# Optimization experiments

Measured on AMD Instinct MI355X. Metric: run time of the kernel, lower is better.

Reference implementation:

```python
import jax, jax.numpy as jnp
import numpy as np

H = 16        # query heads
K = 4         # kv heads (GQA)
D = 128       # head_dim
HID = 2048    # hidden_size
T = 2048      # num tokens (single prefill sequence, causal)
THETA = 10000.0


def setup_inputs() -> dict:
    key = jax.random.key(0)
    k1, k2, k3 = jax.random.split(key, 3)
    hidden_states = jax.random.normal(k1, (T, HID), dtype=jnp.float32)
    position_ids = jnp.arange(T, dtype=jnp.int32)
    Wqkv = jax.random.normal(k2, (HID, (H + 2 * K) * D), dtype=jnp.float32) * 0.02
    Wo = jax.random.normal(k3, (H * D, HID), dtype=jnp.float32) * 0.02
    return {"hidden_states": hidden_states, "position_ids": position_ids,
            "Wqkv": Wqkv, "Wo": Wo}


def _rope_neox(x, pos):
    # x: [T, heads, D]; neox style: rotate halves
    half = D // 2
    inv_freq = 1.0 / (THETA ** (jnp.arange(0, D, 2, dtype=jnp.float32) / D))  # [D/2]
    ang = pos.astype(jnp.float32)[:, None] * inv_freq                          # [T, D/2]
    cos = jnp.cos(ang)[:, None, :]
    sin = jnp.sin(ang)[:, None, :]
    x1, x2 = x[..., :half], x[..., half:]
    return jnp.concatenate([x1 * cos - x2 * sin, x2 * cos + x1 * sin], axis=-1)


def reference(hidden_states, position_ids, Wqkv, Wo):
    t = hidden_states.shape[0]
    qkv = hidden_states @ Wqkv                                   # [T, (H+2K)*D]
    q = qkv[:, : H * D].reshape(t, H, D)
    k = qkv[:, H * D : (H + K) * D].reshape(t, K, D)
    v = qkv[:, (H + K) * D :].reshape(t, K, D)
    q = _rope_neox(q, position_ids)
    k = _rope_neox(k, position_ids)
    # GQA: expand kv heads to H
    rep = H // K
    k = jnp.repeat(k, rep, axis=1)                               # [T, H, D]
    v = jnp.repeat(v, rep, axis=1)
    scale = D ** -0.5
    scores = jnp.einsum('qhd,khd->hqk', q, k) * scale            # [H, T, T]
    causal = jnp.arange(t)[:, None] >= jnp.arange(t)[None, :]    # [T, T]
    scores = jnp.where(causal[None], scores, jnp.finfo(scores.dtype).min)
    probs = jax.nn.softmax(scores, axis=-1)
    ctx = jnp.einsum('hqk,khd->qhd', probs, v).reshape(t, H * D)  # [T, H*D]
    return ctx @ Wo                                              # [T, HID]
```

## Files before the change

kernel.cpp:

```cpp
#include <hip/hip_runtime.h>
#include <hip/hip_bf16.h>
#include <stdint.h>

typedef __hip_bfloat16 bf16;
typedef __attribute__((ext_vector_type(8))) short bh8;
typedef __attribute__((ext_vector_type(4))) float f32x4;

#define MFMA16(a, b, c) __builtin_amdgcn_mfma_f32_16x16x32_bf16((a), (b), (c), 0, 0, 0)

typedef const __attribute__((address_space(1))) void* gas1_t;
typedef __attribute__((address_space(3))) void* las3_t;

__device__ __forceinline__ void gload_lds16(const void* g, void* l) {
  __builtin_amdgcn_global_load_lds((gas1_t)g, (las3_t)l, 16, 0, 0);
}

__device__ __forceinline__ float bfu2f(unsigned short u) {
  union { unsigned int i; float f; } c;
  c.i = (unsigned int)u << 16;
  return c.f;
}

__global__ __launch_bounds__(256) void cast_f32_bf16(const float* __restrict__ x,
                                                     bf16* __restrict__ y, int n4) {
  int i = blockIdx.x * 256 + threadIdx.x;
  if (i >= n4) return;
  float4 v = ((const float4*)x)[i];
  union { ushort4 u; bf16 b[4]; } o;
  o.b[0] = __float2bfloat16(v.x);
  o.b[1] = __float2bfloat16(v.y);
  o.b[2] = __float2bfloat16(v.z);
  o.b[3] = __float2bfloat16(v.w);
  ((ushort4*)y)[i] = o.u;
}

__global__ __launch_bounds__(256) void transpose_cast(const float* __restrict__ W,
                                                      bf16* __restrict__ WT, int R, int C) {
  __shared__ float tile[32][33];
  const int tx = threadIdx.x & 31, ty = threadIdx.x >> 5;
  const int bx = blockIdx.x, by = blockIdx.y;
#pragma unroll
  for (int p = 0; p < 4; ++p)
    tile[ty + p * 8][tx] = W[(long)(by * 32 + ty + p * 8) * C + bx * 32 + tx];
  __syncthreads();
#pragma unroll
  for (int p = 0; p < 4; ++p)
    WT[(long)(bx * 32 + ty + p * 8) * R + by * 32 + tx] = __float2bfloat16(tile[tx][ty + p * 8]);
}

template <bool BF16OUT>
__global__ __launch_bounds__(256) void gemm_bt_sk(const bf16* __restrict__ A,
                                                  const bf16* __restrict__ BT,
                                                  void* __restrict__ C0, void* __restrict__ C1,
                                                  int M, int N, int Kd, int nKs) {
  __shared__ bf16 As[128 * 64];
  __shared__ bf16 Bs[128 * 64];
  const int tid = threadIdx.x, lane = tid & 63, wid = tid >> 6;
  const int wr = wid >> 1, wc = wid & 1;
  const int bx = blockIdx.x, by = blockIdx.y, z = blockIdx.z;

  f32x4 acc[4][4];
#pragma unroll
  for (int m = 0; m < 4; ++m)
#pragma unroll
    for (int n = 0; n < 4; ++n)
#pragma unroll
      for (int r = 0; r < 4; ++r) acc[m][n][r] = 0.0f;

  const long Abase = (long)(by * 128) * Kd;
  const long Bbase = (long)(bx * 128) * Kd;
  const int lr = lane & 15, lh = lane >> 4;
  const int k00 = z * nKs * 64;

  for (int kt = 0; kt < nKs; ++kt) {
    __syncthreads();
    const int k0 = k00 + kt * 64;
#pragma unroll
    for (int i = 0; i < 4; ++i) {
      const int cb = i * 256 + wid * 64;
      const int c = cb + lane;
      const int row = c >> 3, s = c & 7;
      gload_lds16(A + Abase + (long)row * Kd + k0 + (s ^ (row & 7)) * 8, (char*)As + cb * 16);
      gload_lds16(BT + Bbase + (long)row * Kd + k0 + (s ^ (row & 7)) * 8, (char*)Bs + cb * 16);
    }
    __syncthreads();

#pragma unroll
    for (int kk = 0; kk < 2; ++kk) {
      bh8 af[4], bfv[4];
#pragma unroll
      for (int m = 0; m < 4; ++m)
        af[m] = *(const bh8*)((const char*)As +
                              (((wr * 64 + m * 16 + lr) * 128 + kk * 64 + lh * 16) ^
                               ((lr & 7) << 4)));
#pragma unroll
      for (int n = 0; n < 4; ++n)
        bfv[n] = *(const bh8*)((const char*)Bs +
                               (((wc * 64 + n * 16 + lr) * 128 + kk * 64 + lh * 16) ^
                                ((lr & 7) << 4)));
#pragma unroll
      for (int m = 0; m < 4; ++m)
#pragma unroll
        for (int n = 0; n < 4; ++n) acc[m][n] = MFMA16(af[m], bfv[n], acc[m][n]);
    }
  }

  const int r0 = by * 128 + wr * 64, c0 = bx * 128 + wc * 64;
  const int lrow = lh * 4;
  if (BF16OUT) {
    bf16* P = (bf16*)(z == 0 ? C0 : C1);
#pragma unroll
    for (int m = 0; m < 4; ++m)
#pragma unroll
      for (int n = 0; n < 4; ++n)
#pragma unroll
        for (int r = 0; r < 4; ++r)
          P[(long)(r0 + m * 16 + lrow + r) * N + c0 + n * 16 + lr] =
              __float2bfloat16(acc[m][n][r]);
  } else {
    float* P = (float*)(z == 0 ? C0 : C1);
#pragma unroll
    for (int m = 0; m < 4; ++m)
#pragma unroll
      for (int n = 0; n < 4; ++n)
#pragma unroll
        for (int r = 0; r < 4; ++r)
          P[(long)(r0 + m * 16 + lrow + r) * N + c0 + n * 16 + lr] = acc[m][n][r];
  }
}

__global__ __launch_bounds__(256) void out_reduce(float* __restrict__ out,
                                                  const float* __restrict__ p1, int n4) {
  int i = blockIdx.x * 256 + threadIdx.x;
  if (i >= n4) return;
  float4 a = ((const float4*)out)[i];
  float4 b = ((const float4*)p1)[i];
  a.x += b.x; a.y += b.y; a.z += b.z; a.w += b.w;
  ((float4*)out)[i] = a;
}

__global__ __launch_bounds__(256) void rope_split(const bf16* __restrict__ P0,
                                                  const bf16* __restrict__ P1,
                                                  const int* __restrict__ pos_ids,
                                                  bf16* __restrict__ Qb, bf16* __restrict__ Kb,
                                                  bf16* __restrict__ VbT) {
  const int t = blockIdx.x;
  const int tid = threadIdx.x;
  const float pos = (float)pos_ids[t];
  const float qscale = 0.08838834764831845f;
  const ushort* r0 = (const ushort*)(P0 + (long)t * 3072);
  const ushort* r1 = (const ushort*)(P1 + (long)t * 3072);
  for (int i = tid; i < 512; i += 256) {
    const int kvh = i >> 7, d = i & 127;
    const float v = bfu2f(r0[2560 + i]) + bfu2f(r1[2560 + i]);
    VbT[(long)(kvh * 128 + d) * 2048 + t] = __float2bfloat16(v);
  }
  for (int i = tid; i < 1280; i += 256) {
    const int hh = i >> 6, d = i & 63;
    const float inv = exp2f((float)d * -0.2076205059304594f);
    const float ang = pos * inv;
    const float c = cosf(ang), s = sinf(ang);
    const float x1 = bfu2f(r0[hh * 128 + d]) + bfu2f(r1[hh * 128 + d]);
    const float x2 = bfu2f(r0[hh * 128 + d + 64]) + bfu2f(r1[hh * 128 + d + 64]);
    const float o1 = x1 * c - x2 * s, o2 = x2 * c + x1 * s;
    if (hh < 16) {
      Qb[(long)t * 2048 + hh * 128 + d] = __float2bfloat16(o1 * qscale);
      Qb[(long)t * 2048 + hh * 128 + d + 64] = __float2bfloat16(o2 * qscale);
    } else {
      Kb[t * 512 + (hh - 16) * 128 + d] = __float2bfloat16(o1);
      Kb[t * 512 + (hh - 16) * 128 + d + 64] = __float2bfloat16(o2);
    }
  }
}

__global__ __launch_bounds__(256, 2) void attn_partial(const bf16* __restrict__ Qb,
                                                       const bf16* __restrict__ Kb,
                                                       const bf16* __restrict__ VbT,
                                                       bf16* __restrict__ Pctx,
                                                       float* __restrict__ ML) {
  const int h = blockIdx.x;
  const int qb = 31 - blockIdx.y;
  const int z = blockIdx.z;
  const int kh = h >> 2;
  const int tid = threadIdx.x, lane = tid & 63, w = tid >> 6;
  const int pid = (h * 32 + qb) * 2 + z;

  const int nt = qb + 1;
  const int half = (nt + 1) >> 1;
  const int kt0 = z * half;
  const int kt1 = (z == 0) ? half : nt;

  if (kt0 >= kt1) {
    if (tid < 64) {
      ML[pid * 128 + tid] = -1e30f;
      ML[pid * 128 + 64 + tid] = 0.0f;
    }
    ushort4 z4 = make_ushort4(0, 0, 0, 0);
    ushort4* pz = (ushort4*)(Pctx + (long)pid * 8192);
    for (int j = tid; j < 2048; j += 256) pz[j] = z4;
    return;
  }

  __shared__ bf16 Kl[64 * 128];
  __shared__ bf16 Vt[128 * 64];

  const int lr = lane & 15, lh = lane >> 4;
  const int q0w = qb * 64 + w * 16;

  bh8 qf[4];
#pragma unroll
  for (int dc = 0; dc < 4; ++dc)
    qf[dc] = *(const bh8*)&Qb[(long)(q0w + lr) * 2048 + h * 128 + dc * 32 + lh * 8];

  f32x4 ctx[8];
#pragma unroll
  for (int i = 0; i < 8; ++i)
#pragma unroll
    for (int r = 0; r < 4; ++r) ctx[i][r] = 0.0f;
  float mrun = -1e30f, lrun = 0.0f;

  for (int kt = kt0; kt < kt1; ++kt) {
    __syncthreads();
    const long Kbase = ((long)(kt * 64) * 4 + kh) * 128;
#pragma unroll
    for (int i = 0; i < 4; ++i) {
      const int cb = i * 256 + w * 64;
      const int c = cb + lane;
      const int krow = c >> 4, s = c & 15;
      const int g = s ^ ((krow & 3) | ((krow & 8) >> 1));
      gload_lds16(Kb + Kbase + (long)krow * 512 + g * 8, (char*)Kl + cb * 16);
    }
    const long Vbase = (long)kh * 128 * 2048 + kt * 64;
#pragma unroll
    for (int i = 0; i < 4; ++i) {
      const int cb = i * 256 + w * 64;
      const int c = cb + lane;
      const int vrow = c >> 3, s = c & 7;
      gload_lds16(VbT + Vbase + (long)vrow * 2048 + (s ^ (vrow & 7)) * 8, (char*)Vt + cb * 16);
    }
    __syncthreads();

    f32x4 S[2][2];
#pragma unroll
    for (int kc = 0; kc < 2; ++kc)
#pragma unroll
      for (int b = 0; b < 2; ++b) {
#pragma unroll
        for (int r = 0; r < 4; ++r) S[kc][b][r] = 0.0f;
        const int key = kc * 32 + ((lr >> 2) << 3) + b * 4 + (lr & 3);
        const int kbase = key * 256 + lh * 16;
#pragma unroll
        for (int dc = 0; dc < 4; ++dc) {
          bh8 kf = *(const bh8*)((const char*)Kl + ((kbase + dc * 64) ^ ((lr & 7) << 4)));
          S[kc][b] = MFMA16(kf, qf[dc], S[kc][b]);
        }
      }

    if (kt == qb) {
      const int qg = q0w + lr;
#pragma unroll
      for (int kc = 0; kc < 2; ++kc)
#pragma unroll
        for (int b = 0; b < 2; ++b)
#pragma unroll
          for (int r = 0; r < 4; ++r) {
            const int kg = kt * 64 + kc * 32 + lh * 8 + b * 4 + r;
            if (kg > qg) S[kc][b][r] = -1e30f;
          }
    }

    float pm = -1e30f;
#pragma unroll
    for (int kc = 0; kc < 2; ++kc)
#pragma unroll
      for (int b = 0; b < 2; ++b)
#pragma unroll
        for (int r = 0; r < 4; ++r) pm = fmaxf(pm, S[kc][b][r]);
    pm = fmaxf(pm, __shfl_xor(pm, 16, 64));
    pm = fmaxf(pm, __shfl_xor(pm, 32, 64));

    if (__any(pm > mrun + 4.0f)) {
      const float mnew = fmaxf(mrun, pm);
      const float alpha = __expf(mrun - mnew);
      mrun = mnew;
      lrun *= alpha;
      float a4[4];
#pragma unroll
      for (int r = 0; r < 4; ++r) a4[r] = __shfl(alpha, lh * 4 + r, 64);
#pragma unroll
      for (int i = 0; i < 8; ++i)
#pragma unroll
        for (int r = 0; r < 4; ++r) ctx[i][r] *= a4[r];
    }

    bh8 pa[2];
#pragma unroll
    for (int kc = 0; kc < 2; ++kc) {
      union { bh8 v; bf16 e[8]; } pk;
#pragma unroll
      for (int b = 0; b < 2; ++b)
#pragma unroll
        for (int r = 0; r < 4; ++r) {
          const float p = __expf(S[kc][b][r] - mrun);
          lrun += p;
          pk.e[b * 4 + r] = __float2bfloat16(p);
        }
      pa[kc] = pk.v;
    }

#pragma unroll
    for (int kc = 0; kc < 2; ++kc)
#pragma unroll
      for (int dblk = 0; dblk < 8; ++dblk) {
        const int vrow = dblk * 16 + lr;
        const int voff = (vrow * 128 + kc * 64 + lh * 16) ^ ((lr & 7) << 4);
        bh8 vb = *(const bh8*)((const char*)Vt + voff);
        ctx[dblk] = MFMA16(pa[kc], vb, ctx[dblk]);
      }
  }

  float l = lrun;
  l += __shfl_xor(l, 16, 64);
  l += __shfl_xor(l, 32, 64);
  if (lh == 0) {
    ML[pid * 128 + w * 16 + lr] = mrun;
    ML[pid * 128 + 64 + w * 16 + lr] = l;
  }
#pragma unroll
  for (int dblk = 0; dblk < 8; ++dblk)
#pragma unroll
    for (int r = 0; r < 4; ++r)
      Pctx[(long)pid * 8192 + (w * 16 + lh * 4 + r) * 128 + dblk * 16 + lr] =
          __float2bfloat16(ctx[dblk][r]);
}

__global__ __launch_bounds__(256) void attn_merge(const bf16* __restrict__ Pctx,
                                                  const float* __restrict__ ML,
                                                  bf16* __restrict__ out) {
  const int h = blockIdx.x, qb = blockIdx.y;
  const int tid = threadIdx.x;
  const int r = tid >> 2, seg = tid & 3;
  const int pid0 = (h * 32 + qb) * 2;
  const float m0 = ML[pid0 * 128 + r], l0 = ML[pid0 * 128 + 64 + r];
  const float m1 = ML[pid0 * 128 + 128 + r], l1 = ML[pid0 * 128 + 192 + r];
  const float m = fmaxf(m0, m1);
  float a0 = __expf(m0 - m), a1 = __expf(m1 - m);
  const float inv = 1.0f / (l0 * a0 + l1 * a1);
  a0 *= inv;
  a1 *= inv;
  const ushort* p0 = (const ushort*)(Pctx + (long)pid0 * 8192 + r * 128 + seg * 32);
  const ushort* p1 = p0 + 8192;
  bf16* o = out + (long)(qb * 64 + r) * 2048 + h * 128 + seg * 32;
#pragma unroll
  for (int j = 0; j < 4; ++j) {
    union { bh8 v; ushort s[8]; } v0, v1;
    v0.v = *(const bh8*)(p0 + j * 8);
    v1.v = *(const bh8*)(p1 + j * 8);
    union { ushort4 u; bf16 b[4]; } o0, o1;
#pragma unroll
    for (int e = 0; e < 4; ++e) {
      o0.b[e] = __float2bfloat16(bfu2f(v0.s[e]) * a0 + bfu2f(v1.s[e]) * a1);
      o1.b[e] = __float2bfloat16(bfu2f(v0.s[e + 4]) * a0 + bfu2f(v1.s[e + 4]) * a1);
    }
    *(ushort4*)(o + j * 8) = o0.u;
    *(ushort4*)(o + j * 8 + 4) = o1.u;
  }
}

extern "C" void kernel_launch(void* const* d_in, const int* in_sizes, int n_in,
                              void* d_out, int out_size, void* d_ws, size_t ws_size,
                              hipStream_t stream) {
  const float* hs = (const float*)d_in[0];
  const int* pos = (const int*)d_in[1];
  const float* Wqkv = (const float*)d_in[2];
  const float* Wo = (const float*)d_in[3];
  char* ws = (char*)d_ws;

  bf16* hsb = (bf16*)(ws);
  bf16* ctx = (bf16*)(ws);
  bf16* wqkvT = (bf16*)(ws + (8l << 20));
  bf16* Qb = (bf16*)(ws + (8l << 20));
  bf16* Kb = (bf16*)(ws + (16l << 20));
  bf16* VbT = (bf16*)(ws + (18l << 20));
  bf16* woT = (bf16*)(ws + (20l << 20));
  bf16* qkvP0 = (bf16*)(ws + (28l << 20));
  bf16* qkvP1 = (bf16*)(ws + (40l << 20));
  bf16* Pctx = (bf16*)(ws + (28l << 20));
  float* ML = (float*)(ws + (44l << 20));
  float* outP1 = (float*)(ws + (28l << 20));

  cast_f32_bf16<<<4096, 256, 0, stream>>>(hs, hsb, 2048 * 2048 / 4);
  transpose_cast<<<dim3(3072 / 32, 2048 / 32), 256, 0, stream>>>(Wqkv, wqkvT, 2048, 3072);
  transpose_cast<<<dim3(2048 / 32, 2048 / 32), 256, 0, stream>>>(Wo, woT, 2048, 2048);
  gemm_bt_sk<true><<<dim3(24, 16, 2), 256, 0, stream>>>(hsb, wqkvT, qkvP0, qkvP1,
                                                        2048, 3072, 2048, 16);
  rope_split<<<2048, 256, 0, stream>>>(qkvP0, qkvP1, pos, Qb, Kb, VbT);
  attn_partial<<<dim3(16, 32, 2), 256, 0, stream>>>(Qb, Kb, VbT, Pctx, ML);
  attn_merge<<<dim3(16, 32), 256, 0, stream>>>(Pctx, ML, ctx);
  gemm_bt_sk<false><<<dim3(16, 16, 2), 256, 0, stream>>>(ctx, woT, d_out, outP1,
                                                         2048, 2048, 2048, 16);
  out_reduce<<<4096, 256, 0, stream>>>((float*)d_out, outP1, 2048 * 2048 / 4);
}
```

Baseline: 229.9 us.

## Use 4-way split-K with bf16 partials in both GEMMs

Both projection GEMMs now split K four ways instead of two, which raises the number of workgroups to better fill the GPU's compute units. All partials are written as bf16, including the output projection, which previously stored fp32 partials. The rope kernel sums the four partials and computes cos/sin once per token in shared memory. A new reduce kernel sums four bf16 partials into the fp32 output. This adds partial-buffer traffic and rounding error from bf16 partials, and the reduction workload grows.

```diff
diff --git a/kernel.cpp b/kernel.cpp
--- a/kernel.cpp
+++ b/kernel.cpp
@@ -48,11 +48,11 @@
     WT[(long)(bx * 32 + ty + p * 8) * R + by * 32 + tx] = __float2bfloat16(tile[tx][ty + p * 8]);
 }
 
-template <bool BF16OUT>
-__global__ __launch_bounds__(256) void gemm_bt_sk(const bf16* __restrict__ A,
-                                                  const bf16* __restrict__ BT,
-                                                  void* __restrict__ C0, void* __restrict__ C1,
-                                                  int M, int N, int Kd, int nKs) {
+__global__ __launch_bounds__(256) void gemm_bt_sk4(const bf16* __restrict__ A,
+                                                   const bf16* __restrict__ BT,
+                                                   bf16* __restrict__ c0, bf16* __restrict__ c1,
+                                                   bf16* __restrict__ c2, bf16* __restrict__ c3,
+                                                   int M, int N, int Kd, int nKs) {
   __shared__ bf16 As[128 * 64];
   __shared__ bf16 Bs[128 * 64];
   const int tid = threadIdx.x, lane = tid & 63, wid = tid >> 6;
@@ -105,63 +105,83 @@
     }
   }
 
-  const int r0 = by * 128 + wr * 64, c0 = bx * 128 + wc * 64;
+  bf16* P = (z == 0) ? c0 : (z == 1) ? c1 : (z == 2) ? c2 : c3;
+  const int r0 = by * 128 + wr * 64, c0i = bx * 128 + wc * 64;
   const int lrow = lh * 4;
-  if (BF16OUT) {
-    bf16* P = (bf16*)(z == 0 ? C0 : C1);
-#pragma unroll
-    for (int m = 0; m < 4; ++m)
-#pragma unroll
-      for (int n = 0; n < 4; ++n)
-#pragma unroll
-        for (int r = 0; r < 4; ++r)
-          P[(long)(r0 + m * 16 + lrow + r) * N + c0 + n * 16 + lr] =
-              __float2bfloat16(acc[m][n][r]);
-  } else {
-    float* P = (float*)(z == 0 ? C0 : C1);
-#pragma unroll
-    for (int m = 0; m < 4; ++m)
-#pragma unroll
-      for (int n = 0; n < 4; ++n)
-#pragma unroll
-        for (int r = 0; r < 4; ++r)
-          P[(long)(r0 + m * 16 + lrow + r) * N + c0 + n * 16 + lr] = acc[m][n][r];
-  }
-}
-
-__global__ __launch_bounds__(256) void out_reduce(float* __restrict__ out,
-                                                  const float* __restrict__ p1, int n4) {
+#pragma unroll
+  for (int m = 0; m < 4; ++m)
+#pragma unroll
+    for (int n = 0; n < 4; ++n)
+#pragma unroll
+      for (int r = 0; r < 4; ++r)
+        P[(long)(r0 + m * 16 + lrow + r) * N + c0i + n * 16 + lr] =
+            __float2bfloat16(acc[m][n][r]);
+}
+
+__global__ __launch_bounds__(256) void out_reduce4(float* __restrict__ out,
+                                                   const bf16* __restrict__ p0,
+                                                   const bf16* __restrict__ p1,
+                                                   const bf16* __restrict__ p2,
+                                                   const bf16* __restrict__ p3, int n8) {
   int i = blockIdx.x * 256 + threadIdx.x;
-  if (i >= n4) return;
-  float4 a = ((const float4*)out)[i];
-  float4 b = ((const float4*)p1)[i];
-  a.x += b.x; a.y += b.y; a.z += b.z; a.w += b.w;
-  ((float4*)out)[i] = a;
+  if (i >= n8) return;
+  union { bh8 v; ushort s[8]; } a, b, c, d;
+  a.v = *(const bh8*)(p0 + (long)i * 8);
+  b.v = *(const bh8*)(p1 + (long)i * 8);
+  c.v = *(const bh8*)(p2 + (long)i * 8);
+  d.v = *(const bh8*)(p3 + (long)i * 8);
+  float4 o0, o1;
+  float* oo = &o0.x;
+#pragma unroll
+  for (int e = 0; e < 8; ++e) {
+    const float f = bfu2f(a.s[e]) + bfu2f(b.s[e]) + bfu2f(c.s[e]) + bfu2f(d.s[e]);
+    if (e < 4) (&o0.x)[e] = f; else (&o1.x)[e - 4] = f;
+  }
+  (void)oo;
+  ((float4*)out)[i * 2] = o0;
+  ((float4*)out)[i * 2 + 1] = o1;
 }
 
 __global__ __launch_bounds__(256) void rope_split(const bf16* __restrict__ P0,
                                                   const bf16* __restrict__ P1,
+                                                  const bf16* __restrict__ P2,
+                                                  const bf16* __restrict__ P3,
                                                   const int* __restrict__ pos_ids,
                                                   bf16* __restrict__ Qb, bf16* __restrict__ Kb,
                                                   bf16* __restrict__ VbT) {
+  __shared__ float lcs[64], lsn[64];
   const int t = blockIdx.x;
   const int tid = threadIdx.x;
   const float pos = (float)pos_ids[t];
   const float qscale = 0.08838834764831845f;
   const ushort* r0 = (const ushort*)(P0 + (long)t * 3072);
   const ushort* r1 = (const ushort*)(P1 + (long)t * 3072);
+  const ushort* r2 = (const ushort*)(P2 + (long)t * 3072);
+  const ushort* r3 = (const ushort*)(P3 + (long)t * 3072);
+
+  if (tid < 64) {
+    const float inv = exp2f((float)tid * -0.2076205059304594f);
+    const float ang = pos * inv;
+    float s, c;
+    __sincosf(ang, &s, &c);
+    lcs[tid] = c;
+    lsn[tid] = s;
+  }
+  __syncthreads();
+
   for (int i = tid; i < 512; i += 256) {
     const int kvh = i >> 7, d = i & 127;
-    const float v = bfu2f(r0[2560 + i]) + bfu2f(r1[2560 + i]);
+    const float v = bfu2f(r0[2560 + i]) + bfu2f(r1[2560 + i]) + bfu2f(r2[2560 + i]) +
+                    bfu2f(r3[2560 + i]);
     VbT[(long)(kvh * 128 + d) * 2048 + t] = __float2bfloat16(v);
   }
   for (int i = tid; i < 1280; i += 256) {
     const int hh = i >> 6, d = i & 63;
-    const float inv = exp2f((float)d * -0.2076205059304594f);
-    const float ang = pos * inv;
-    const float c = cosf(ang), s = sinf(ang);
-    const float x1 = bfu2f(r0[hh * 128 + d]) + bfu2f(r1[hh * 128 + d]);
-    const float x2 = bfu2f(r0[hh * 128 + d + 64]) + bfu2f(r1[hh * 128 + d + 64]);
+    const float c = lcs[d], s = lsn[d];
+    const float x1 = bfu2f(r0[hh * 128 + d]) + bfu2f(r1[hh * 128 + d]) +
+                     bfu2f(r2[hh * 128 + d]) + bfu2f(r3[hh * 128 + d]);
+    const float x2 = bfu2f(r0[hh * 128 + d + 64]) + bfu2f(r1[hh * 128 + d + 64]) +
+                     bfu2f(r2[hh * 128 + d + 64]) + bfu2f(r3[hh * 128 + d + 64]);
     const float o1 = x1 * c - x2 * s, o2 = x2 * c + x1 * s;
     if (hh < 16) {
       Qb[(long)t * 2048 + hh * 128 + d] = __float2bfloat16(o1 * qscale);
@@ -385,19 +405,24 @@
   bf16* woT = (bf16*)(ws + (20l << 20));
   bf16* qkvP0 = (bf16*)(ws + (28l << 20));
   bf16* qkvP1 = (bf16*)(ws + (40l << 20));
+  bf16* qkvP2 = (bf16*)(ws + (52l << 20));
+  bf16* qkvP3 = (bf16*)(ws + (64l << 20));
   bf16* Pctx = (bf16*)(ws + (28l << 20));
   float* ML = (float*)(ws + (44l << 20));
-  float* outP1 = (float*)(ws + (28l << 20));
+  bf16* oP0 = (bf16*)(ws + (48l << 20));
+  bf16* oP1 = (bf16*)(ws + (56l << 20));
+  bf16* oP2 = (bf16*)(ws + (64l << 20));
+  bf16* oP3 = (bf16*)(ws + (72l << 20));
 
   cast_f32_bf16<<<4096, 256, 0, stream>>>(hs, hsb, 2048 * 2048 / 4);
   transpose_cast<<<dim3(3072 / 32, 2048 / 32), 256, 0, stream>>>(Wqkv, wqkvT, 2048, 3072);
   transpose_cast<<<dim3(2048 / 32, 2048 / 32), 256, 0, stream>>>(Wo, woT, 2048, 2048);
-  gemm_bt_sk<true><<<dim3(24, 16, 2), 256, 0, stream>>>(hsb, wqkvT, qkvP0, qkvP1,
-                                                        2048, 3072, 2048, 16);
-  rope_split<<<2048, 256, 0, stream>>>(qkvP0, qkvP1, pos, Qb, Kb, VbT);
+  gemm_bt_sk4<<<dim3(24, 16, 4), 256, 0, stream>>>(hsb, wqkvT, qkvP0, qkvP1, qkvP2, qkvP3,
+                                                   2048, 3072, 2048, 8);
+  rope_split<<<2048, 256, 0, stream>>>(qkvP0, qkvP1, qkvP2, qkvP3, pos, Qb, Kb, VbT);
   attn_partial<<<dim3(16, 32, 2), 256, 0, stream>>>(Qb, Kb, VbT, Pctx, ML);
   attn_merge<<<dim3(16, 32), 256, 0, stream>>>(Pctx, ML, ctx);
-  gemm_bt_sk<false><<<dim3(16, 16, 2), 256, 0, stream>>>(ctx, woT, d_out, outP1,
-                                                         2048, 2048, 2048, 16);
-  out_reduce<<<4096, 256, 0, stream>>>((float*)d_out, outP1, 2048 * 2048 / 4);
-}
+  gemm_bt_sk4<<<dim3(16, 16, 4), 256, 0, stream>>>(ctx, woT, oP0, oP1, oP2, oP3,
+                                                   2048, 2048, 2048, 8);
+  out_reduce4<<<2048, 256, 0, stream>>>((float*)d_out, oP0, oP1, oP2, oP3, 2048 * 2048 / 8);
+}
```

Measured after the change: 232.7 us. Within noise of the previous version (+1.2%).

## Double-buffer LDS tiles in GEMM and attention, precompute RoPE sin/cos in shared memory

Applied to the files above, without the earlier changes.

Adds two-stage LDS double buffering to both the bf16 GEMM and the attention partial kernel, so the next K/V or A/B tile is fetched with global_load_lds while the current tile is consumed by MFMAs. This drops one barrier per iteration. The rope kernel now computes the 64 sin/cos values once per token into shared memory with __sincosf instead of recomputing cosf/sinf per element. The cost is double the LDS footprint (64KB for the GEMM, 64KB for attention), which may reduce occupancy. There is also a correctness question: the loop relies on the end-of-iteration barrier to make the prefetched async LDS writes visible, with no explicit vmcnt wait.

```diff
diff --git a/kernel.cpp b/kernel.cpp
--- a/kernel.cpp
+++ b/kernel.cpp
@@ -53,8 +53,8 @@
                                                   const bf16* __restrict__ BT,
                                                   void* __restrict__ C0, void* __restrict__ C1,
                                                   int M, int N, int Kd, int nKs) {
-  __shared__ bf16 As[128 * 64];
-  __shared__ bf16 Bs[128 * 64];
+  __shared__ bf16 As[2][128 * 64];
+  __shared__ bf16 Bs[2][128 * 64];
   const int tid = threadIdx.x, lane = tid & 63, wid = tid >> 6;
   const int wr = wid >> 1, wc = wid & 1;
   const int bx = blockIdx.x, by = blockIdx.y, z = blockIdx.z;
@@ -72,40 +72,49 @@
   const int lr = lane & 15, lh = lane >> 4;
   const int k00 = z * nKs * 64;
 
+#define G_STAGE(BUF, KT)                                                                   \
+  {                                                                                        \
+    const int k0 = k00 + (KT) * 64;                                                        \
+    _Pragma("unroll") for (int i = 0; i < 4; ++i) {                                        \
+      const int cb = i * 256 + wid * 64;                                                   \
+      const int c = cb + lane;                                                             \
+      const int row = c >> 3, s = c & 7;                                                   \
+      gload_lds16(A + Abase + (long)row * Kd + k0 + (s ^ (row & 7)) * 8,                   \
+                  (char*)As[BUF] + cb * 16);                                               \
+      gload_lds16(BT + Bbase + (long)row * Kd + k0 + (s ^ (row & 7)) * 8,                  \
+                  (char*)Bs[BUF] + cb * 16);                                               \
+    }                                                                                      \
+  }
+
+  G_STAGE(0, 0);
+  __syncthreads();
+  int cur = 0;
   for (int kt = 0; kt < nKs; ++kt) {
-    __syncthreads();
-    const int k0 = k00 + kt * 64;
-#pragma unroll
-    for (int i = 0; i < 4; ++i) {
-      const int cb = i * 256 + wid * 64;
-      const int c = cb + lane;
-      const int row = c >> 3, s = c & 7;
-      gload_lds16(A + Abase + (long)row * Kd + k0 + (s ^ (row & 7)) * 8, (char*)As + cb * 16);
-      gload_lds16(BT + Bbase + (long)row * Kd + k0 + (s ^ (row & 7)) * 8, (char*)Bs + cb * 16);
-    }
-    __syncthreads();
-
+    if (kt + 1 < nKs) G_STAGE(cur ^ 1, kt + 1);
+    const char* Ab = (const char*)As[cur];
+    const char* Bb = (const char*)Bs[cur];
 #pragma unroll
     for (int kk = 0; kk < 2; ++kk) {
       bh8 af[4], bfv[4];
 #pragma unroll
       for (int m = 0; m < 4; ++m)
-        af[m] = *(const bh8*)((const char*)As +
-                              (((wr * 64 + m * 16 + lr) * 128 + kk * 64 + lh * 16) ^
-                               ((lr & 7) << 4)));
+        af[m] = *(const bh8*)(Ab + (((wr * 64 + m * 16 + lr) * 128 + kk * 64 + lh * 16) ^
+                                    ((lr & 7) << 4)));
 #pragma unroll
       for (int n = 0; n < 4; ++n)
-        bfv[n] = *(const bh8*)((const char*)Bs +
-                               (((wc * 64 + n * 16 + lr) * 128 + kk * 64 + lh * 16) ^
-                                ((lr & 7) << 4)));
+        bfv[n] = *(const bh8*)(Bb + (((wc * 64 + n * 16 + lr) * 128 + kk * 64 + lh * 16) ^
+                                     ((lr & 7) << 4)));
 #pragma unroll
       for (int m = 0; m < 4; ++m)
 #pragma unroll
         for (int n = 0; n < 4; ++n) acc[m][n] = MFMA16(af[m], bfv[n], acc[m][n]);
     }
-  }
-
-  const int r0 = by * 128 + wr * 64, c0 = bx * 128 + wc * 64;
+    __syncthreads();
+    cur ^= 1;
+  }
+#undef G_STAGE
+
+  const int r0 = by * 128 + wr * 64, c0i = bx * 128 + wc * 64;
   const int lrow = lh * 4;
   if (BF16OUT) {
     bf16* P = (bf16*)(z == 0 ? C0 : C1);
@@ -115,7 +124,7 @@
       for (int n = 0; n < 4; ++n)
 #pragma unroll
         for (int r = 0; r < 4; ++r)
-          P[(long)(r0 + m * 16 + lrow + r) * N + c0 + n * 16 + lr] =
+          P[(long)(r0 + m * 16 + lrow + r) * N + c0i + n * 16 + lr] =
               __float2bfloat16(acc[m][n][r]);
   } else {
     float* P = (float*)(z == 0 ? C0 : C1);
@@ -125,7 +134,7 @@
       for (int n = 0; n < 4; ++n)
 #pragma unroll
         for (int r = 0; r < 4; ++r)
-          P[(long)(r0 + m * 16 + lrow + r) * N + c0 + n * 16 + lr] = acc[m][n][r];
+          P[(long)(r0 + m * 16 + lrow + r) * N + c0i + n * 16 + lr] = acc[m][n][r];
   }
 }
 
@@ -144,12 +153,23 @@
                                                   const int* __restrict__ pos_ids,
                                                   bf16* __restrict__ Qb, bf16* __restrict__ Kb,
                                                   bf16* __restrict__ VbT) {
+  __shared__ float lcs[64], lsn[64];
   const int t = blockIdx.x;
   const int tid = threadIdx.x;
   const float pos = (float)pos_ids[t];
   const float qscale = 0.08838834764831845f;
   const ushort* r0 = (const ushort*)(P0 + (long)t * 3072);
   const ushort* r1 = (const ushort*)(P1 + (long)t * 3072);
+
+  if (tid < 64) {
+    const float inv = exp2f((float)tid * -0.2076205059304594f);
+    float s, c;
+    __sincosf(pos * inv, &s, &c);
+    lcs[tid] = c;
+    lsn[tid] = s;
+  }
+  __syncthreads();
+
   for (int i = tid; i < 512; i += 256) {
     const int kvh = i >> 7, d = i & 127;
     const float v = bfu2f(r0[2560 + i]) + bfu2f(r1[2560 + i]);
@@ -157,9 +177,7 @@
   }
   for (int i = tid; i < 1280; i += 256) {
     const int hh = i >> 6, d = i & 63;
-    const float inv = exp2f((float)d * -0.2076205059304594f);
-    const float ang = pos * inv;
-    const float c = cosf(ang), s = sinf(ang);
+    const float c = lcs[d], s = lsn[d];
     const float x1 = bfu2f(r0[hh * 128 + d]) + bfu2f(r1[hh * 128 + d]);
     const float x2 = bfu2f(r0[hh * 128 + d + 64]) + bfu2f(r1[hh * 128 + d + 64]);
     const float o1 = x1 * c - x2 * s, o2 = x2 * c + x1 * s;
@@ -201,12 +219,32 @@
     return;
   }
 
-  __shared__ bf16 Kl[64 * 128];
-  __shared__ bf16 Vt[128 * 64];
+  __shared__ bf16 Kl[2][64 * 128];
+  __shared__ bf16 Vt[2][128 * 64];
 
   const int lr = lane & 15, lh = lane >> 4;
   const int q0w = qb * 64 + w * 16;
 
+#define KV_STAGE(BUF, KT)                                                                  \
+  {                                                                                        \
+    const long Kbase = ((long)((KT) * 64) * 4 + kh) * 128;                                 \
+    _Pragma("unroll") for (int i = 0; i < 4; ++i) {                                        \
+      const int cb = i * 256 + w * 64;                                                     \
+      const int c = cb + lane;                                                             \
+      const int krow = c >> 4, s = c & 15;                                                 \
+      const int g = s ^ ((krow & 3) | ((krow & 8) >> 1));                                  \
+      gload_lds16(Kb + Kbase + (long)krow * 512 + g * 8, (char*)Kl[BUF] + cb * 16);        \
+    }                                                                                      \
+    const long Vbase = (long)kh * 128 * 2048 + (KT) * 64;                                  \
+    _Pragma("unroll") for (int i = 0; i < 4; ++i) {                                        \
+      const int cb = i * 256 + w * 64;                                                     \
+      const int c = cb + lane;                                                             \
+      const int vrow = c >> 3, s = c & 7;                                                  \
+      gload_lds16(VbT + Vbase + (long)vrow * 2048 + (s ^ (vrow & 7)) * 8,                  \
+                  (char*)Vt[BUF] + cb * 16);                                               \
+    }                                                                                      \
+  }
+
   bh8 qf[4];
 #pragma unroll
   for (int dc = 0; dc < 4; ++dc)
@@ -219,26 +257,13 @@
     for (int r = 0; r < 4; ++r) ctx[i][r] = 0.0f;
   float mrun = -1e30f, lrun = 0.0f;
 
+  KV_STAGE(0, kt0);
+  __syncthreads();
+  int cur = 0;
   for (int kt = kt0; kt < kt1; ++kt) {
-    __syncthreads();
-    const long Kbase = ((long)(kt * 64) * 4 + kh) * 128;
-#pragma unroll
-    for (int i = 0; i < 4; ++i) {
-      const int cb = i * 256 + w * 64;
-      const int c = cb + lane;
-      const int krow = c >> 4, s = c & 15;
-      const int g = s ^ ((krow & 3) | ((krow & 8) >> 1));
-      gload_lds16(Kb + Kbase + (long)krow * 512 + g * 8, (char*)Kl + cb * 16);
-    }
-    const long Vbase = (long)kh * 128 * 2048 + kt * 64;
-#pragma unroll
-    for (int i = 0; i < 4; ++i) {
-      const int cb = i * 256 + w * 64;
-      const int c = cb + lane;
-      const int vrow = c >> 3, s = c & 7;
-      gload_lds16(VbT + Vbase + (long)vrow * 2048 + (s ^ (vrow & 7)) * 8, (char*)Vt + cb * 16);
-    }
-    __syncthreads();
+    if (kt + 1 < kt1) KV_STAGE(cur ^ 1, kt + 1);
+    const char* Kc = (const char*)Kl[cur];
+    const char* Vc = (const char*)Vt[cur];
 
     f32x4 S[2][2];
 #pragma unroll
@@ -251,7 +276,7 @@
         const int kbase = key * 256 + lh * 16;
 #pragma unroll
         for (int dc = 0; dc < 4; ++dc) {
-          bh8 kf = *(const bh8*)((const char*)Kl + ((kbase + dc * 64) ^ ((lr & 7) << 4)));
+          bh8 kf = *(const bh8*)(Kc + ((kbase + dc * 64) ^ ((lr & 7) << 4)));
           S[kc][b] = MFMA16(kf, qf[dc], S[kc][b]);
         }
       }
@@ -314,10 +339,14 @@
       for (int dblk = 0; dblk < 8; ++dblk) {
         const int vrow = dblk * 16 + lr;
         const int voff = (vrow * 128 + kc * 64 + lh * 16) ^ ((lr & 7) << 4);
-        bh8 vb = *(const bh8*)((const char*)Vt + voff);
+        bh8 vb = *(const bh8*)(Vc + voff);
         ctx[dblk] = MFMA16(pa[kc], vb, ctx[dblk]);
       }
-  }
+
+    __syncthreads();
+    cur ^= 1;
+  }
+#undef KV_STAGE
 
   float l = lrun;
   l += __shfl_xor(l, 16, 64);
```

New measurement: 225.7 us. No clear change (-1.8%).
